# Kernel optimization log

Measured on AMD Instinct MI355X. Metric: run time of the kernel, lower is better.

Reference implementation:

```python
import jax, jax.numpy as jnp
import numpy as np

NUM_HEAD = 16
DIM = 1024
T, B = 2048, 4


def setup_inputs() -> dict:
    key = jax.random.key(0)
    ks = jax.random.split(key, 12)
    s = 1.0 / np.sqrt(DIM)
    return {
        "x1": jax.random.normal(ks[0], (T, B, DIM), jnp.float32),
        "x2": jax.random.normal(ks[1], (T, B, DIM), jnp.float32),
        "Wq": jax.random.normal(ks[2], (DIM, DIM), jnp.float32) * s,
        "bq": jax.random.normal(ks[3], (DIM,), jnp.float32) * 0.01,
        "Wk": jax.random.normal(ks[4], (DIM, DIM), jnp.float32) * s,
        "bk": jax.random.normal(ks[5], (DIM,), jnp.float32) * 0.01,
        "Wv": jax.random.normal(ks[6], (DIM, DIM), jnp.float32) * s,
        "bv": jax.random.normal(ks[7], (DIM,), jnp.float32) * 0.01,
        "Wu": jax.random.normal(ks[8], (DIM, DIM), jnp.float32) * s,
        "bu": jax.random.normal(ks[9], (DIM,), jnp.float32) * 0.01,
    }


def reference(x1, x2, Wq, bq, Wk, bk, Wv, bv, Wu, bu):
    T1, B1, C = x1.shape
    T2 = x2.shape[0]
    H = NUM_HEAD
    hd = C // H
    # (T,B,C) -> (B,T,C)
    x1b = jnp.transpose(x1, (1, 0, 2))
    x2b = jnp.transpose(x2, (1, 0, 2))
    # torch Linear: y = x @ W.T + b
    q = (x1b @ Wq.T + bq).reshape(B1, T1, H, hd).transpose(0, 2, 1, 3)  # (B,H,T1,hd)
    k = (x2b @ Wk.T + bk).reshape(B1, T2, H, hd).transpose(0, 2, 1, 3)
    v = (x2b @ Wv.T + bv).reshape(B1, T2, H, hd).transpose(0, 2, 1, 3)
    # NOTE: source scales by 1/sqrt(C) (full dim), not 1/sqrt(head_dim)
    attn = jnp.einsum("bhqd,bhkd->bhqk", q, k) / jnp.sqrt(jnp.asarray(C, q.dtype))
    attn = jax.nn.softmax(attn, axis=-1)
    # dropout = identity (eval mode, deterministic reference)
    out = jnp.einsum("bhqk,bhkd->bhqd", attn, v)  # (B,H,T1,hd)
    out = out.transpose(0, 2, 1, 3).reshape(B1, T1, C)  # merge heads
    out = out @ Wu.T + bu
    return out
```

## Files before the change

kernel.cpp:

```cpp
#include <hip/hip_runtime.h>

#define TSEQ 2048
#define BB 4
#define CDIM 1024
#define NH 16
#define HD 64
#define MR (TSEQ*BB)
#define C2SCALE 0.045084220f

typedef __attribute__((ext_vector_type(8))) short sh8;
typedef __attribute__((ext_vector_type(4))) short sh4;
typedef __attribute__((ext_vector_type(4))) float f4;

__device__ __forceinline__ unsigned short f2bf(float x){
  unsigned u = __builtin_bit_cast(unsigned, x);
  u += 0x7fffu + ((u>>16)&1u);
  return (unsigned short)(u>>16);
}

__device__ __forceinline__ unsigned pk2(float a, float b){
  unsigned ua = __builtin_bit_cast(unsigned, a) + 0x8000u;
  unsigned ub = __builtin_bit_cast(unsigned, b) + 0x8000u;
  return __builtin_amdgcn_perm(ua, ub, 0x07060302u);
}

__device__ __forceinline__ void gll16(const unsigned short* g, unsigned short* l){
  __builtin_amdgcn_global_load_lds(
      (const __attribute__((address_space(1))) unsigned int*)g,
      (__attribute__((address_space(3))) unsigned int*)l, 16, 0, 0);
}

__global__ void conv_x(const float* __restrict__ a, const float* __restrict__ b,
                       unsigned short* __restrict__ ya, unsigned short* __restrict__ yb){
  const float* s = blockIdx.y ? b : a;
  unsigned short* d = blockIdx.y ? yb : ya;
  int i = (blockIdx.x*256 + threadIdx.x)*4;
  f4 v = *(const f4*)(s+i);
  sh4 o;
  o.x = (short)f2bf(v.x); o.y = (short)f2bf(v.y);
  o.z = (short)f2bf(v.z); o.w = (short)f2bf(v.w);
  *(sh4*)(d+i) = o;
}

__global__ void conv_w(const float* __restrict__ w0, const float* __restrict__ w1,
                       const float* __restrict__ w2, const float* __restrict__ w3,
                       unsigned short* __restrict__ y0, unsigned short* __restrict__ y1,
                       unsigned short* __restrict__ y2, unsigned short* __restrict__ y3){
  const float* s; unsigned short* d;
  switch(blockIdx.y){
    case 0: s=w0; d=y0; break;
    case 1: s=w1; d=y1; break;
    case 2: s=w2; d=y2; break;
    default: s=w3; d=y3; break;
  }
  int i = (blockIdx.x*256 + threadIdx.x)*4;
  f4 v = *(const f4*)(s+i);
  sh4 o;
  o.x = (short)f2bf(v.x); o.y = (short)f2bf(v.y);
  o.z = (short)f2bf(v.z); o.w = (short)f2bf(v.w);
  *(sh4*)(d+i) = o;
}

template<int MODE>
__global__ __launch_bounds__(256,2) void gemm_bt(
    const unsigned short* __restrict__ A, const unsigned short* __restrict__ Bw,
    const float* __restrict__ bias, void* __restrict__ Cout){
  __shared__ unsigned short As[128*32];
  __shared__ unsigned short Bs[128*32];
  const int tid  = threadIdx.x;
  const int wave = tid>>6, lane = tid&63;
  const int g = lane>>4, c = lane&15;
  const int m0 = blockIdx.x*128, n0 = blockIdx.y*128;
  const int wr = wave>>1, wc = wave&1;
  f4 acc[4][4] = {};
  const int r0 = tid>>2, cc0 = tid&3;
  const unsigned short* Ag = A  + (size_t)(m0+r0)*CDIM + cc0*8;
  const unsigned short* Bg = Bw + (size_t)(n0+r0)*CDIM + cc0*8;

  for (int k0=0; k0<CDIM; k0+=32){
    __syncthreads();
    gll16(Ag + k0,                    As + tid*8);
    gll16(Ag + (size_t)64*CDIM + k0,  As + (256+tid)*8);
    gll16(Bg + k0,                    Bs + tid*8);
    gll16(Bg + (size_t)64*CDIM + k0,  Bs + (256+tid)*8);
    __syncthreads();
    sh8 af[4], bfr[4];
#pragma unroll
    for (int mt=0; mt<4; mt++) af[mt]  = *(const sh8*)(As + (wr*64+mt*16+c)*32 + g*8);
#pragma unroll
    for (int nt=0; nt<4; nt++) bfr[nt] = *(const sh8*)(Bs + (wc*64+nt*16+c)*32 + g*8);
#pragma unroll
    for (int mt=0; mt<4; mt++)
#pragma unroll
      for (int nt=0; nt<4; nt++)
        acc[mt][nt] = __builtin_amdgcn_mfma_f32_16x16x32_bf16(af[mt], bfr[nt], acc[mt][nt], 0,0,0);
  }

#pragma unroll
  for (int nt=0; nt<4; nt++){
    int nn = n0 + wc*64 + nt*16 + c;
    float bsv = bias[nn];
#pragma unroll
    for (int mt=0; mt<4; mt++){
      int mb = m0 + wr*64 + mt*16 + 4*g;
#pragma unroll
      for (int r=0; r<4; r++){
        float v = acc[mt][nt][r] + bsv;
        int mm = mb + r;
        if (MODE==0 || MODE==3){
          float vv = (MODE==3) ? v*C2SCALE : v;
          ((unsigned short*)Cout)[(size_t)mm*CDIM + nn] = f2bf(vv);
        } else if (MODE==1){
          int t = mm>>2, bb = mm&3, h = nn>>6, d = nn&63;
          ((unsigned short*)Cout)[(((size_t)bb*NH + h)*HD + d)*TSEQ + t] = f2bf(v);
        } else {
          ((float*)Cout)[(size_t)mm*CDIM + nn] = v;
        }
      }
    }
  }
}

__global__ __launch_bounds__(256,2) void gemm_kv(
    const unsigned short* __restrict__ A,
    const unsigned short* __restrict__ Bk, const unsigned short* __restrict__ Bv,
    const float* __restrict__ biask, const float* __restrict__ biasv,
    unsigned short* __restrict__ Kout, unsigned short* __restrict__ Vout){
  __shared__ unsigned short As[128*32];
  __shared__ unsigned short Bs1[128*32];
  __shared__ unsigned short Bs2[128*32];
  const int tid  = threadIdx.x;
  const int wave = tid>>6, lane = tid&63;
  const int g = lane>>4, c = lane&15;
  const int m0 = blockIdx.x*128, n0 = blockIdx.y*128;
  const int wr = wave>>1, wc = wave&1;
  f4 acck[4][4] = {}, accv[4][4] = {};
  const int r0 = tid>>2, cc0 = tid&3;
  const unsigned short* Ag  = A  + (size_t)(m0+r0)*CDIM + cc0*8;
  const unsigned short* Bkg = Bk + (size_t)(n0+r0)*CDIM + cc0*8;
  const unsigned short* Bvg = Bv + (size_t)(n0+r0)*CDIM + cc0*8;

  for (int k0=0; k0<CDIM; k0+=32){
    __syncthreads();
    gll16(Ag  + k0,                    As  + tid*8);
    gll16(Ag  + (size_t)64*CDIM + k0,  As  + (256+tid)*8);
    gll16(Bkg + k0,                    Bs1 + tid*8);
    gll16(Bkg + (size_t)64*CDIM + k0,  Bs1 + (256+tid)*8);
    gll16(Bvg + k0,                    Bs2 + tid*8);
    gll16(Bvg + (size_t)64*CDIM + k0,  Bs2 + (256+tid)*8);
    __syncthreads();
    sh8 af[4], bk4[4], bv4[4];
#pragma unroll
    for (int mt=0; mt<4; mt++) af[mt]  = *(const sh8*)(As  + (wr*64+mt*16+c)*32 + g*8);
#pragma unroll
    for (int nt=0; nt<4; nt++) bk4[nt] = *(const sh8*)(Bs1 + (wc*64+nt*16+c)*32 + g*8);
#pragma unroll
    for (int nt=0; nt<4; nt++) bv4[nt] = *(const sh8*)(Bs2 + (wc*64+nt*16+c)*32 + g*8);
#pragma unroll
    for (int mt=0; mt<4; mt++)
#pragma unroll
      for (int nt=0; nt<4; nt++){
        acck[mt][nt] = __builtin_amdgcn_mfma_f32_16x16x32_bf16(af[mt], bk4[nt], acck[mt][nt], 0,0,0);
        accv[mt][nt] = __builtin_amdgcn_mfma_f32_16x16x32_bf16(af[mt], bv4[nt], accv[mt][nt], 0,0,0);
      }
  }

#pragma unroll
  for (int nt=0; nt<4; nt++){
    int nn = n0 + wc*64 + nt*16 + c;
    float bkv = biask[nn], bvv = biasv[nn];
#pragma unroll
    for (int mt=0; mt<4; mt++){
      int mb = m0 + wr*64 + mt*16 + 4*g;
#pragma unroll
      for (int r=0; r<4; r++){
        int mm = mb + r;
        Kout[(size_t)mm*CDIM + nn] = f2bf(acck[mt][nt][r] + bkv);
        int t = mm>>2, bb = mm&3, h = nn>>6, d = nn&63;
        Vout[(((size_t)bb*NH + h)*HD + d)*TSEQ + t] = f2bf(accv[mt][nt][r] + bvv);
      }
    }
  }
}

__global__ __launch_bounds__(256,3) void attn_kernel(
    const unsigned short* __restrict__ Q, const unsigned short* __restrict__ Kb,
    const unsigned short* __restrict__ Vt, unsigned short* __restrict__ O){
  __shared__ unsigned short Ks[128*64];
  __shared__ unsigned short Vs[64*128];
  __shared__ unsigned short Ps[4][32*64];
  const int tid=threadIdx.x, wave=tid>>6, lane=tid&63;
  const int g=lane>>4, c=lane&15;
  const int qt=blockIdx.x, bh=blockIdx.y, b=bh>>4, h=bh&15;
  const int qbase = qt*128 + wave*32;

  sh8 qfr[2][2];
#pragma unroll
  for (int qf=0; qf<2; qf++)
#pragma unroll
    for (int kc=0; kc<2; kc++){
      int t = qbase + qf*16 + c;
      qfr[qf][kc] = *(const sh8*)(Q + ((size_t)t*BB + b)*CDIM + h*HD + kc*32 + g*8);
    }

  f4 oacc[4][2] = {};
  float lrun[2] = {0.f, 0.f};

  for (int k0=0; k0<TSEQ; k0+=128){
    __syncthreads();
#pragma unroll
    for (int i=0; i<4; i++){
      int cc = i*256+tid, row = cc>>3, ch = (cc&7) ^ (row&7);
      gll16(Kb + ((size_t)(k0+row)*BB + b)*CDIM + h*HD + ch*8, Ks + cc*8);
    }
#pragma unroll
    for (int i=0; i<4; i++){
      int cc = i*256+tid, d = cc>>4, ch = (cc&15) ^ (d&15);
      gll16(Vt + ((size_t)(b*NH+h)*HD + d)*TSEQ + k0 + ch*8, Vs + cc*8);
    }
    __syncthreads();

    f4 sacc[8][2] = {};
#pragma unroll
    for (int kf=0; kf<8; kf++){
      sh8 af[2];
#pragma unroll
      for (int kc=0; kc<2; kc++){
        int ch = (kc*4+g) ^ (c&7);
        af[kc] = *(const sh8*)(Ks + (kf*16+c)*64 + ch*8);
      }
#pragma unroll
      for (int kc=0; kc<2; kc++)
#pragma unroll
        for (int qf=0; qf<2; qf++)
          sacc[kf][qf] = __builtin_amdgcn_mfma_f32_16x16x32_bf16(af[kc], qfr[qf][kc], sacc[kf][qf],0,0,0);
    }

#pragma unroll
    for (int half=0; half<2; half++){
#pragma unroll
      for (int qf=0; qf<2; qf++){
        unsigned short* prow = Ps[wave] + (qf*16+c)*64;
#pragma unroll
        for (int kfl=0; kfl<4; kfl++){
          int kf = half*4 + kfl;
          float p0 = __builtin_amdgcn_exp2f(sacc[kf][qf][0]);
          float p1 = __builtin_amdgcn_exp2f(sacc[kf][qf][1]);
          float p2 = __builtin_amdgcn_exp2f(sacc[kf][qf][2]);
          float p3 = __builtin_amdgcn_exp2f(sacc[kf][qf][3]);
          lrun[qf] += (p0+p1)+(p2+p3);
          unsigned d0 = pk2(p1, p0);
          unsigned d1 = pk2(p3, p2);
          int js = (kfl*4+g) ^ (c&14);
          uint2 pr; pr.x = d0; pr.y = d1;
          *(uint2*)(prow + js*4) = pr;
        }
      }
#pragma unroll
      for (int kc2l=0; kc2l<2; kc2l++){
        int kc2 = half*2 + kc2l;
        sh8 pf[2];
#pragma unroll
        for (int qf=0; qf<2; qf++){
          int j0 = kc2l*8 + 2*g;
          pf[qf] = *(const sh8*)(Ps[wave] + (qf*16+c)*64 + ((j0 ^ (c&14)))*4);
        }
#pragma unroll
        for (int df=0; df<4; df++){
          int ch = (kc2*4+g) ^ c;
          sh8 vf = *(const sh8*)(Vs + (df*16+c)*128 + ch*8);
#pragma unroll
          for (int qf=0; qf<2; qf++)
            oacc[df][qf] = __builtin_amdgcn_mfma_f32_16x16x32_bf16(vf, pf[qf], oacc[df][qf],0,0,0);
        }
      }
    }
  }

#pragma unroll
  for (int qf=0; qf<2; qf++){
    lrun[qf] += __shfl_xor(lrun[qf], 16, 64);
    lrun[qf] += __shfl_xor(lrun[qf], 32, 64);
    float inv = 1.0f/lrun[qf];
    int t = qbase + qf*16 + c;
#pragma unroll
    for (int df=0; df<4; df++){
      uint2 pr;
      pr.x = pk2(oacc[df][qf][1]*inv, oacc[df][qf][0]*inv);
      pr.y = pk2(oacc[df][qf][3]*inv, oacc[df][qf][2]*inv);
      *(uint2*)(O + ((size_t)b*TSEQ + t)*CDIM + h*HD + df*16 + 4*g) = pr;
    }
  }
}

extern "C" void kernel_launch(void* const* d_in, const int* in_sizes, int n_in,
                              void* d_out, int out_size, void* d_ws, size_t ws_size,
                              hipStream_t stream){
  (void)in_sizes; (void)n_in; (void)out_size; (void)ws_size;
  const float* x1 = (const float*)d_in[0];
  const float* x2 = (const float*)d_in[1];
  const float* Wq = (const float*)d_in[2];
  const float* bq = (const float*)d_in[3];
  const float* Wk = (const float*)d_in[4];
  const float* bk = (const float*)d_in[5];
  const float* Wv = (const float*)d_in[6];
  const float* bv = (const float*)d_in[7];
  const float* Wu = (const float*)d_in[8];
  const float* bu = (const float*)d_in[9];

  unsigned short* ws = (unsigned short*)d_ws;
  size_t o = 0;
  unsigned short* x1b = ws + o; o += (size_t)MR*CDIM;
  unsigned short* x2b = ws + o; o += (size_t)MR*CDIM;
  unsigned short* wqb = ws + o; o += (size_t)CDIM*CDIM;
  unsigned short* wkb = ws + o; o += (size_t)CDIM*CDIM;
  unsigned short* wvb = ws + o; o += (size_t)CDIM*CDIM;
  unsigned short* wub = ws + o; o += (size_t)CDIM*CDIM;
  unsigned short* Qb  = ws + o; o += (size_t)MR*CDIM;
  unsigned short* Kbf = ws + o; o += (size_t)MR*CDIM;
  unsigned short* Vtb = ws + o; o += (size_t)MR*CDIM;
  unsigned short* Ob  = x1b;

  conv_x<<<dim3((MR*CDIM)/1024, 2),   256, 0, stream>>>(x1, x2, x1b, x2b);
  conv_w<<<dim3((CDIM*CDIM)/1024, 4), 256, 0, stream>>>(Wq, Wk, Wv, Wu, wqb, wkb, wvb, wub);

  dim3 gg(MR/128, CDIM/128);
  gemm_bt<3><<<gg, 256, 0, stream>>>(x1b, wqb, bq, Qb);
  gemm_kv  <<<gg, 256, 0, stream>>>(x2b, wkb, wvb, bk, bv, Kbf, Vtb);
  attn_kernel<<<dim3(TSEQ/128, BB*NH), 256, 0, stream>>>(Qb, Kbf, Vtb, Ob);
  gemm_bt<2><<<gg, 256, 0, stream>>>(Ob, wub, bu, (float*)d_out);
}
```

Measured before the change: 367.3 us.

## Double query tile per attention block to reuse K/V tiles, remap grid

Each attention workgroup now handles two 128-row query tiles (256 queries) per load of a K/V tile from shared memory. This halves the global-to-LDS K/V traffic and the sync count per query. The launch becomes a 1D grid of 512 blocks, with a swizzled mapping that groups blocks sharing the same head so L2 reuse improves. The cost is more registers and doubled P scratch in LDS, which drops occupancy from 3 to 2 blocks per CU. Unused GEMM modes are also removed.

After: 449.4 us. +22.3%, slower.

```diff
diff --git a/kernel.cpp b/kernel.cpp
--- a/kernel.cpp
+++ b/kernel.cpp
@@ -107,12 +107,8 @@
       for (int r=0; r<4; r++){
         float v = acc[mt][nt][r] + bsv;
         int mm = mb + r;
-        if (MODE==0 || MODE==3){
-          float vv = (MODE==3) ? v*C2SCALE : v;
-          ((unsigned short*)Cout)[(size_t)mm*CDIM + nn] = f2bf(vv);
-        } else if (MODE==1){
-          int t = mm>>2, bb = mm&3, h = nn>>6, d = nn&63;
-          ((unsigned short*)Cout)[(((size_t)bb*NH + h)*HD + d)*TSEQ + t] = f2bf(v);
+        if (MODE==3){
+          ((unsigned short*)Cout)[(size_t)mm*CDIM + nn] = f2bf(v*C2SCALE);
         } else {
           ((float*)Cout)[(size_t)mm*CDIM + nn] = v;
         }
@@ -183,28 +179,32 @@
   }
 }
 
-__global__ __launch_bounds__(256,3) void attn_kernel(
+__global__ __launch_bounds__(256,2) void attn_kernel(
     const unsigned short* __restrict__ Q, const unsigned short* __restrict__ Kb,
     const unsigned short* __restrict__ Vt, unsigned short* __restrict__ O){
   __shared__ unsigned short Ks[128*64];
   __shared__ unsigned short Vs[64*128];
-  __shared__ unsigned short Ps[4][32*64];
+  __shared__ unsigned short Ps[4][2][32*64];
   const int tid=threadIdx.x, wave=tid>>6, lane=tid&63;
   const int g=lane>>4, c=lane&15;
-  const int qt=blockIdx.x, bh=blockIdx.y, b=bh>>4, h=bh&15;
-  const int qbase = qt*128 + wave*32;
-
-  sh8 qfr[2][2];
-#pragma unroll
-  for (int qf=0; qf<2; qf++)
-#pragma unroll
-    for (int kc=0; kc<2; kc++){
-      int t = qbase + qf*16 + c;
-      qfr[qf][kc] = *(const sh8*)(Q + ((size_t)t*BB + b)*CDIM + h*HD + kc*32 + g*8);
-    }
-
-  f4 oacc[4][2] = {};
-  float lrun[2] = {0.f, 0.f};
+  const int gx = blockIdx.x;
+  const int bh = ((gx>>6)<<3) | (gx&7);
+  const int qt = (gx>>3)&7;
+  const int b = bh>>4, h = bh&15;
+
+  sh8 qfr[2][2][2];
+#pragma unroll
+  for (int qtile=0; qtile<2; qtile++)
+#pragma unroll
+    for (int qf=0; qf<2; qf++)
+#pragma unroll
+      for (int kc=0; kc<2; kc++){
+        int t = qt*256 + qtile*128 + wave*32 + qf*16 + c;
+        qfr[qtile][qf][kc] = *(const sh8*)(Q + ((size_t)t*BB + b)*CDIM + h*HD + kc*32 + g*8);
+      }
+
+  f4 oacc[2][4][2] = {};
+  float lrun[2][2] = {};
 
   for (int k0=0; k0<TSEQ; k0+=128){
     __syncthreads();
@@ -220,77 +220,89 @@
     }
     __syncthreads();
 
-    f4 sacc[8][2] = {};
-#pragma unroll
-    for (int kf=0; kf<8; kf++){
-      sh8 af[2];
-#pragma unroll
-      for (int kc=0; kc<2; kc++){
-        int ch = (kc*4+g) ^ (c&7);
-        af[kc] = *(const sh8*)(Ks + (kf*16+c)*64 + ch*8);
-      }
-#pragma unroll
-      for (int kc=0; kc<2; kc++)
-#pragma unroll
-        for (int qf=0; qf<2; qf++)
-          sacc[kf][qf] = __builtin_amdgcn_mfma_f32_16x16x32_bf16(af[kc], qfr[qf][kc], sacc[kf][qf],0,0,0);
-    }
-
 #pragma unroll
     for (int half=0; half<2; half++){
-#pragma unroll
-      for (int qf=0; qf<2; qf++){
-        unsigned short* prow = Ps[wave] + (qf*16+c)*64;
-#pragma unroll
-        for (int kfl=0; kfl<4; kfl++){
-          int kf = half*4 + kfl;
-          float p0 = __builtin_amdgcn_exp2f(sacc[kf][qf][0]);
-          float p1 = __builtin_amdgcn_exp2f(sacc[kf][qf][1]);
-          float p2 = __builtin_amdgcn_exp2f(sacc[kf][qf][2]);
-          float p3 = __builtin_amdgcn_exp2f(sacc[kf][qf][3]);
-          lrun[qf] += (p0+p1)+(p2+p3);
-          unsigned d0 = pk2(p1, p0);
-          unsigned d1 = pk2(p3, p2);
-          int js = (kfl*4+g) ^ (c&14);
-          uint2 pr; pr.x = d0; pr.y = d1;
-          *(uint2*)(prow + js*4) = pr;
+      f4 sacc[2][4][2] = {};
+#pragma unroll
+      for (int kfl=0; kfl<4; kfl++){
+        int kf = half*4 + kfl;
+        sh8 af[2];
+#pragma unroll
+        for (int kc=0; kc<2; kc++){
+          int ch = (kc*4+g) ^ (c&7);
+          af[kc] = *(const sh8*)(Ks + (kf*16+c)*64 + ch*8);
         }
-      }
+#pragma unroll
+        for (int qtile=0; qtile<2; qtile++)
+#pragma unroll
+          for (int kc=0; kc<2; kc++)
+#pragma unroll
+            for (int qf=0; qf<2; qf++)
+              sacc[qtile][kfl][qf] = __builtin_amdgcn_mfma_f32_16x16x32_bf16(
+                  af[kc], qfr[qtile][qf][kc], sacc[qtile][kfl][qf],0,0,0);
+      }
+
+#pragma unroll
+      for (int qtile=0; qtile<2; qtile++)
+#pragma unroll
+        for (int qf=0; qf<2; qf++){
+          unsigned short* prow = Ps[wave][qtile] + (qf*16+c)*64;
+#pragma unroll
+          for (int kfl=0; kfl<4; kfl++){
+            float p0 = __builtin_amdgcn_exp2f(sacc[qtile][kfl][qf][0]);
+            float p1 = __builtin_amdgcn_exp2f(sacc[qtile][kfl][qf][1]);
+            float p2 = __builtin_amdgcn_exp2f(sacc[qtile][kfl][qf][2]);
+            float p3 = __builtin_amdgcn_exp2f(sacc[qtile][kfl][qf][3]);
+            lrun[qtile][qf] += (p0+p1)+(p2+p3);
+            uint2 pr; pr.x = pk2(p1, p0); pr.y = pk2(p3, p2);
+            int js = (kfl*4+g) ^ (c&14);
+            *(uint2*)(prow + js*4) = pr;
+          }
+        }
+
 #pragma unroll
       for (int kc2l=0; kc2l<2; kc2l++){
         int kc2 = half*2 + kc2l;
-        sh8 pf[2];
-#pragma unroll
-        for (int qf=0; qf<2; qf++){
-          int j0 = kc2l*8 + 2*g;
-          pf[qf] = *(const sh8*)(Ps[wave] + (qf*16+c)*64 + ((j0 ^ (c&14)))*4);
-        }
+        sh8 pf[2][2];
+#pragma unroll
+        for (int qtile=0; qtile<2; qtile++)
+#pragma unroll
+          for (int qf=0; qf<2; qf++){
+            int j0 = kc2l*8 + 2*g;
+            pf[qtile][qf] = *(const sh8*)(Ps[wave][qtile] + (qf*16+c)*64 + (j0^(c&14))*4);
+          }
 #pragma unroll
         for (int df=0; df<4; df++){
           int ch = (kc2*4+g) ^ c;
           sh8 vf = *(const sh8*)(Vs + (df*16+c)*128 + ch*8);
 #pragma unroll
-          for (int qf=0; qf<2; qf++)
-            oacc[df][qf] = __builtin_amdgcn_mfma_f32_16x16x32_bf16(vf, pf[qf], oacc[df][qf],0,0,0);
+          for (int qtile=0; qtile<2; qtile++)
+#pragma unroll
+            for (int qf=0; qf<2; qf++)
+              oacc[qtile][df][qf] = __builtin_amdgcn_mfma_f32_16x16x32_bf16(
+                  vf, pf[qtile][qf], oacc[qtile][df][qf],0,0,0);
         }
       }
     }
   }
 
 #pragma unroll
-  for (int qf=0; qf<2; qf++){
-    lrun[qf] += __shfl_xor(lrun[qf], 16, 64);
-    lrun[qf] += __shfl_xor(lrun[qf], 32, 64);
-    float inv = 1.0f/lrun[qf];
-    int t = qbase + qf*16 + c;
-#pragma unroll
-    for (int df=0; df<4; df++){
-      uint2 pr;
-      pr.x = pk2(oacc[df][qf][1]*inv, oacc[df][qf][0]*inv);
-      pr.y = pk2(oacc[df][qf][3]*inv, oacc[df][qf][2]*inv);
-      *(uint2*)(O + ((size_t)b*TSEQ + t)*CDIM + h*HD + df*16 + 4*g) = pr;
-    }
-  }
+  for (int qtile=0; qtile<2; qtile++)
+#pragma unroll
+    for (int qf=0; qf<2; qf++){
+      float l = lrun[qtile][qf];
+      l += __shfl_xor(l, 16, 64);
+      l += __shfl_xor(l, 32, 64);
+      float inv = 1.0f/l;
+      int t = qt*256 + qtile*128 + wave*32 + qf*16 + c;
+#pragma unroll
+      for (int df=0; df<4; df++){
+        uint2 pr;
+        pr.x = pk2(oacc[qtile][df][qf][1]*inv, oacc[qtile][df][qf][0]*inv);
+        pr.y = pk2(oacc[qtile][df][qf][3]*inv, oacc[qtile][df][qf][2]*inv);
+        *(uint2*)(O + ((size_t)b*TSEQ + t)*CDIM + h*HD + df*16 + 4*g) = pr;
+      }
+    }
 }
 
 extern "C" void kernel_launch(void* const* d_in, const int* in_sizes, int n_in,
@@ -327,6 +339,6 @@
   dim3 gg(MR/128, CDIM/128);
   gemm_bt<3><<<gg, 256, 0, stream>>>(x1b, wqb, bq, Qb);
   gemm_kv  <<<gg, 256, 0, stream>>>(x2b, wkb, wvb, bk, bv, Kbf, Vtb);
-  attn_kernel<<<dim3(TSEQ/128, BB*NH), 256, 0, stream>>>(Qb, Kbf, Vtb, Ob);
+  attn_kernel<<<dim3(512), 256, 0, stream>>>(Qb, Kbf, Vtb, Ob);
   gemm_bt<2><<<gg, 256, 0, stream>>>(Ob, wub, bu, (float*)d_out);
 }
```
